# Performance work log

Hardware: AMD Instinct MI355X
Metric: run time of the kernel (lower is better)

## Reference

```python
import jax, jax.numpy as jnp
import numpy as np

B, N, D, H, M, CD = 2, 2048, 1024, 16, 77, 768
DH = D // H          # head dim 64
FF = 4 * D           # GEGLU hidden 4096
NBITS = 8
EPS = 1e-5


def fake_quant_w(w, n_bits=NBITS):
    """Per-tensor uniform affine INT8 fake-quant (UniformAffineQuantizerINT8) with STE."""
    levels = 2 ** n_bits - 1
    mn = jnp.min(w)
    mx = jnp.max(w)
    delta = (mx - mn) / levels
    zp = jnp.round(-mn / delta)
    wq = jnp.clip(jnp.round(w / delta) + zp, 0, levels)
    wdq = (wq - zp) * delta
    return w + jax.lax.stop_gradient(wdq - w)


def layernorm(x, g, b):
    mu = jnp.mean(x, axis=-1, keepdims=True)
    var = jnp.mean((x - mu) ** 2, axis=-1, keepdims=True)
    return (x - mu) * jax.lax.rsqrt(var + EPS) * g + b


def linear(x, w, b=None):
    y = x @ fake_quant_w(w).T
    return y if b is None else y + b


def cross_attn(x, ctx, qw, kw, vw, ow, ob):
    Bq, Nq, _ = x.shape
    Nk = ctx.shape[1]
    q = linear(x, qw).reshape(Bq, Nq, H, DH)     # b n h d
    k = linear(ctx, kw).reshape(Bq, Nk, H, DH)
    v = linear(ctx, vw).reshape(Bq, Nk, H, DH)
    scale = DH ** -0.5
    sim = jnp.einsum('bihd,bjhd->bhij', q, k) * scale   # [B,H,Nq,Nk]
    attn = jax.nn.softmax(sim, axis=-1)
    out = jnp.einsum('bhij,bjhd->bihd', attn, v).reshape(Bq, Nq, D)
    return linear(out, ow, ob)


def geglu_ff(x, w1, b1, w2, b2):
    h = linear(x, w1, b1)                # [B,N,2*FF]
    hidden, gate = jnp.split(h, 2, axis=-1)
    return linear(hidden * jax.nn.gelu(gate), w2, b2)


def setup_inputs() -> dict:
    key = jax.random.key(0)
    ks = jax.random.split(key, 24)
    W = lambda k, o, i: (jax.random.normal(k, (o, i), jnp.float32) * 0.02)
    return {
        'x': jax.random.normal(ks[0], (B, N, D), jnp.float32),
        'context': jax.random.normal(ks[1], (B, M, CD), jnp.float32),
        'ln1_g': 1.0 + 0.1 * jax.random.normal(ks[2], (D,), jnp.float32),
        'ln1_b': 0.1 * jax.random.normal(ks[3], (D,), jnp.float32),
        'ln2_g': 1.0 + 0.1 * jax.random.normal(ks[4], (D,), jnp.float32),
        'ln2_b': 0.1 * jax.random.normal(ks[5], (D,), jnp.float32),
        'ln3_g': 1.0 + 0.1 * jax.random.normal(ks[6], (D,), jnp.float32),
        'ln3_b': 0.1 * jax.random.normal(ks[7], (D,), jnp.float32),
        'q1_w': W(ks[8], D, D), 'k1_w': W(ks[9], D, D), 'v1_w': W(ks[10], D, D),
        'o1_w': W(ks[11], D, D), 'o1_b': jnp.zeros((D,), jnp.float32),
        'q2_w': W(ks[12], D, D), 'k2_w': W(ks[13], D, CD), 'v2_w': W(ks[14], D, CD),
        'o2_w': W(ks[15], D, D), 'o2_b': jnp.zeros((D,), jnp.float32),
        'ff1_w': W(ks[16], 2 * FF, D), 'ff1_b': jnp.zeros((2 * FF,), jnp.float32),
        'ff2_w': W(ks[17], D, FF), 'ff2_b': jnp.zeros((D,), jnp.float32),
    }


def reference(x, context, ln1_g, ln1_b, ln2_g, ln2_b, ln3_g, ln3_b,
              q1_w, k1_w, v1_w, o1_w, o1_b,
              q2_w, k2_w, v2_w, o2_w, o2_b,
              ff1_w, ff1_b, ff2_w, ff2_b):
    x = cross_attn(layernorm(x, ln1_g, ln1_b), layernorm(x, ln1_g, ln1_b),
                   q1_w, k1_w, v1_w, o1_w, o1_b) + x
    x = cross_attn(layernorm(x, ln2_g, ln2_b), context,
                   q2_w, k2_w, v2_w, o2_w, o2_b) + x
    x = geglu_ff(layernorm(x, ln3_g, ln3_b), ff1_w, ff1_b, ff2_w, ff2_b) + x
    return x
```

## Files before the change

kernel.cpp:

```cpp
#include <hip/hip_runtime.h>
#include <cstdint>
#include <cstddef>

typedef unsigned short ushort_t;
typedef short s16x8 __attribute__((ext_vector_type(8)));
typedef float f32x4 __attribute__((ext_vector_type(4)));
typedef unsigned u32x4 __attribute__((ext_vector_type(4)));

#define MFMA(A,B,C) __builtin_amdgcn_mfma_f32_16x16x32_bf16((A),(B),(C),0,0,0)

__device__ __forceinline__ float b2f(ushort_t h){ return __uint_as_float(((unsigned)h)<<16); }
__device__ __forceinline__ ushort_t f2b(float f){
  unsigned u = __float_as_uint(f);
  u += 0x7FFFu + ((u >> 16) & 1u);
  return (ushort_t)(u >> 16);
}
__device__ __forceinline__ unsigned f2o(float f){
  unsigned u = __float_as_uint(f);
  return (u & 0x80000000u) ? ~u : (u | 0x80000000u);
}
__device__ __forceinline__ float o2f(unsigned u){
  unsigned b = (u & 0x80000000u) ? (u & 0x7FFFFFFFu) : ~u;
  return __uint_as_float(b);
}

struct QT { const float* w[10]; ushort_t* o[10]; int n[10]; };

__global__ void init_k(unsigned* slots){
  int t = threadIdx.x;
  if (t < 20) slots[t] = (t & 1) ? 0u : 0xFFFFFFFFu;
}

__global__ __launch_bounds__(256) void minmax_k(QT qt, unsigned* slots){
  int t = blockIdx.y;
  const float4* w = (const float4*)qt.w[t];
  int n4 = qt.n[t] >> 2;
  float mn = 3.4e38f, mx = -3.4e38f;
  for (int i = blockIdx.x*256 + threadIdx.x; i < n4; i += gridDim.x*256){
    float4 v = w[i];
    mn = fminf(mn, fminf(fminf(v.x, v.y), fminf(v.z, v.w)));
    mx = fmaxf(mx, fmaxf(fmaxf(v.x, v.y), fmaxf(v.z, v.w)));
  }
  #pragma unroll
  for (int o = 1; o < 64; o <<= 1){
    mn = fminf(mn, __shfl_xor(mn, o));
    mx = fmaxf(mx, __shfl_xor(mx, o));
  }
  __shared__ float smn[4], smx[4];
  int wv = threadIdx.x >> 6;
  if ((threadIdx.x & 63) == 0){ smn[wv] = mn; smx[wv] = mx; }
  __syncthreads();
  if (threadIdx.x == 0){
    mn = fminf(fminf(smn[0], smn[1]), fminf(smn[2], smn[3]));
    mx = fmaxf(fmaxf(smx[0], smx[1]), fmaxf(smx[2], smx[3]));
    atomicMin(&slots[2*t], f2o(mn));
    atomicMax(&slots[2*t+1], f2o(mx));
  }
}

__global__ __launch_bounds__(256) void dequant_k(QT qt, const unsigned* __restrict__ slots){
  int t = blockIdx.y;
  float mn = o2f(slots[2*t]), mx = o2f(slots[2*t+1]);
  float delta = (mx - mn) * (1.f/255.f);
  float zp = rintf(-mn / delta);
  const float4* w = (const float4*)qt.w[t];
  ushort4* o = (ushort4*)qt.o[t];
  int n4 = qt.n[t] >> 2;
  for (int i = blockIdx.x*256 + threadIdx.x; i < n4; i += gridDim.x*256){
    float4 v = w[i];
    ushort4 r;
    float q;
    q = fminf(fmaxf(rintf(v.x/delta) + zp, 0.f), 255.f); r.x = f2b((q - zp)*delta);
    q = fminf(fmaxf(rintf(v.y/delta) + zp, 0.f), 255.f); r.y = f2b((q - zp)*delta);
    q = fminf(fmaxf(rintf(v.z/delta) + zp, 0.f), 255.f); r.z = f2b((q - zp)*delta);
    q = fminf(fmaxf(rintf(v.w/delta) + zp, 0.f), 255.f); r.w = f2b((q - zp)*delta);
    o[i] = r;
  }
}

__global__ __launch_bounds__(256) void f2b_k(const float* __restrict__ in, ushort_t* __restrict__ out, int n4){
  for (int i = blockIdx.x*256 + threadIdx.x; i < n4; i += gridDim.x*256){
    float4 v = ((const float4*)in)[i];
    ushort4 r; r.x = f2b(v.x); r.y = f2b(v.y); r.z = f2b(v.z); r.w = f2b(v.w);
    ((ushort4*)out)[i] = r;
  }
}

__global__ __launch_bounds__(256) void ln_k(const float* __restrict__ x, const float* __restrict__ g,
                                            const float* __restrict__ b, ushort_t* __restrict__ out){
  int row = blockIdx.x, tid = threadIdx.x;
  float4 v = ((const float4*)(x + (size_t)row*1024))[tid];
  float s  = v.x + v.y + v.z + v.w;
  float s2 = v.x*v.x + v.y*v.y + v.z*v.z + v.w*v.w;
  #pragma unroll
  for (int o = 1; o < 64; o <<= 1){ s += __shfl_xor(s, o); s2 += __shfl_xor(s2, o); }
  __shared__ float rs[4], rs2[4];
  int wv = tid >> 6;
  if ((tid & 63) == 0){ rs[wv] = s; rs2[wv] = s2; }
  __syncthreads();
  s = rs[0]+rs[1]+rs[2]+rs[3]; s2 = rs2[0]+rs2[1]+rs2[2]+rs2[3];
  float mu = s * (1.f/1024.f);
  float var = s2 * (1.f/1024.f) - mu*mu;
  float rstd = rsqrtf(var + 1e-5f);
  float4 gv = ((const float4*)g)[tid], bv = ((const float4*)b)[tid];
  ushort4 r;
  r.x = f2b((v.x - mu)*rstd*gv.x + bv.x);
  r.y = f2b((v.y - mu)*rstd*gv.y + bv.y);
  r.z = f2b((v.z - mu)*rstd*gv.z + bv.z);
  r.w = f2b((v.w - mu)*rstd*gv.w + bv.w);
  ((ushort4*)(out + (size_t)row*1024))[tid] = r;
}

__global__ __launch_bounds__(256) void gemm_k(
    const ushort_t* __restrict__ A, const ushort_t* __restrict__ W,
    const float* __restrict__ bias, const float* __restrict__ resid,
    float* __restrict__ outF, ushort_t* __restrict__ outB,
    int M, int N, int K, int lda, int ldw)
{
  __shared__ ushort_t As[3][128*32];
  __shared__ ushort_t Bs[3][128*32];
  const int tid = threadIdx.x;
  const int lane = tid & 63, wv = tid >> 6;
  const int g = lane >> 4, qi = lane & 15;

  const int gx = gridDim.x, gy = gridDim.y;
  const int lid = blockIdx.x + blockIdx.y * gx;
  const int w = gx >> 2, h = gy >> 1;
  const int xcd = lid & 7, o = lid >> 3;
  const int cx = xcd & 3, cy = xcd >> 2;
  const int n0 = (cx * w + (o % w)) * 128;
  const int m0 = (cy * h + (o / w)) * 128;

  const int koff = blockIdx.z * K;
  if (gridDim.z > 1) outF += (size_t)blockIdx.z * M * N;

  const int wr = (wv >> 1) * 64, wc = (wv & 1) * 64;
  f32x4 acc[4][4] = {};

  const int r0 = tid >> 2,        s0 = (tid & 3) ^ ((r0 >> 1) & 3);
  const int r1 = (256+tid) >> 2,  s1 = ((256+tid) & 3) ^ ((r1 >> 1) & 3);
  const int ar0 = (m0 + r0 < M) ? m0 + r0 : M - 1;
  const int ar1 = (m0 + r1 < M) ? m0 + r1 : M - 1;
  const size_t dst0 = (size_t)(wv*64)*8, dst1 = (size_t)(256 + wv*64)*8;

  #define GSTAGE(bi_, kt_) do {                                                    \
    __builtin_amdgcn_global_load_lds(                                              \
      (const __attribute__((address_space(1))) void*)(A + (size_t)ar0*lda + koff + (kt_) + s0*8), \
      (__attribute__((address_space(3))) void*)(&As[bi_][dst0]), 16, 0, 0);        \
    __builtin_amdgcn_global_load_lds(                                              \
      (const __attribute__((address_space(1))) void*)(W + (size_t)(n0 + r0)*ldw + koff + (kt_) + s0*8), \
      (__attribute__((address_space(3))) void*)(&Bs[bi_][dst0]), 16, 0, 0);        \
    __builtin_amdgcn_global_load_lds(                                              \
      (const __attribute__((address_space(1))) void*)(A + (size_t)ar1*lda + koff + (kt_) + s1*8), \
      (__attribute__((address_space(3))) void*)(&As[bi_][dst1]), 16, 0, 0);        \
    __builtin_amdgcn_global_load_lds(                                              \
      (const __attribute__((address_space(1))) void*)(W + (size_t)(n0 + r1)*ldw + koff + (kt_) + s1*8), \
      (__attribute__((address_space(3))) void*)(&Bs[bi_][dst1]), 16, 0, 0);        \
  } while(0)

  const int nt = K >> 5;
  GSTAGE(0, 0);
  if (nt > 1) GSTAGE(1, 32);
  if (nt > 1) asm volatile("s_waitcnt vmcnt(4)" ::: "memory");
  else        asm volatile("s_waitcnt vmcnt(0)" ::: "memory");
  __builtin_amdgcn_s_barrier();
  __builtin_amdgcn_sched_barrier(0);

  int bi = 0;
  for (int t = 0; t < nt; ++t){
    int b2 = bi + 2; if (b2 >= 3) b2 -= 3;
    if (t + 2 < nt) GSTAGE(b2, (t + 2) << 5);
    s16x8 af[4], bfr[4];
    #pragma unroll
    for (int mi = 0; mi < 4; ++mi){
      int row = wr + mi*16 + qi;
      int sl = g ^ ((row >> 1) & 3);
      af[mi] = *(const s16x8*)(&As[bi][row*32 + sl*8]);
    }
    #pragma unroll
    for (int ni = 0; ni < 4; ++ni){
      int row = wc + ni*16 + qi;
      int sl = g ^ ((row >> 1) & 3);
      bfr[ni] = *(const s16x8*)(&Bs[bi][row*32 + sl*8]);
    }
    __builtin_amdgcn_s_setprio(1);
    #pragma unroll
    for (int mi = 0; mi < 4; ++mi)
      #pragma unroll
      for (int ni = 0; ni < 4; ++ni)
        acc[mi][ni] = MFMA(af[mi], bfr[ni], acc[mi][ni]);
    __builtin_amdgcn_s_setprio(0);
    if (t + 1 < nt){
      if (t + 2 < nt) asm volatile("s_waitcnt vmcnt(4)" ::: "memory");
      else            asm volatile("s_waitcnt vmcnt(0)" ::: "memory");
      __builtin_amdgcn_s_barrier();
      __builtin_amdgcn_sched_barrier(0);
    }
    bi += 1; if (bi >= 3) bi -= 3;
  }
  #undef GSTAGE

  #pragma unroll
  for (int mi = 0; mi < 4; ++mi){
    #pragma unroll
    for (int r = 0; r < 4; ++r){
      int row = m0 + wr + mi*16 + g*4 + r;
      if (row >= M) continue;
      #pragma unroll
      for (int ni = 0; ni < 4; ++ni){
        int col = n0 + wc + ni*16 + qi;
        float v = acc[mi][ni][r];
        if (bias)  v += bias[col];
        if (resid) v += resid[(size_t)row*N + col];
        if (outF)  outF[(size_t)row*N + col] = v;
        else       outB[(size_t)row*N + col] = f2b(v);
      }
    }
  }
}

__global__ __launch_bounds__(256) void reduce_k(const float* __restrict__ p0, const float* __restrict__ p1,
                                                const float* __restrict__ bias, const float* __restrict__ resid,
                                                float* __restrict__ outF, ushort_t* __restrict__ outB, int n4){
  for (int i = blockIdx.x*256 + threadIdx.x; i < n4; i += gridDim.x*256){
    float4 a = ((const float4*)p0)[i];
    float4 b = ((const float4*)p1)[i];
    float4 v;
    v.x = a.x + b.x; v.y = a.y + b.y; v.z = a.z + b.z; v.w = a.w + b.w;
    if (bias){
      float4 bb = ((const float4*)bias)[i & 255];
      v.x += bb.x; v.y += bb.y; v.z += bb.z; v.w += bb.w;
    }
    if (resid){
      float4 r = ((const float4*)resid)[i];
      v.x += r.x; v.y += r.y; v.z += r.z; v.w += r.w;
    }
    if (outF) ((float4*)outF)[i] = v;
    else {
      ushort4 o; o.x = f2b(v.x); o.y = f2b(v.y); o.z = f2b(v.z); o.w = f2b(v.w);
      ((ushort4*)outB)[i] = o;
    }
  }
}

__global__ __launch_bounds__(256) void vtrans_k(const ushort_t* __restrict__ src, ushort_t* __restrict__ dst,
                                                int rows, int stride, int col_off, int nk_pad){
  __shared__ ushort_t ldst[64*130];
  int n0 = blockIdx.x * 128;
  int b = blockIdx.y >> 4, h = blockIdx.y & 15;
  const ushort_t* s = src + (size_t)b*rows*stride + col_off + h*64;
  for (int idx = threadIdx.x; idx < 128*64; idx += 256){
    int n = idx >> 6, d = idx & 63;
    int ng = n0 + n;
    ushort_t v = (ng < rows) ? s[(size_t)ng*stride + d] : (ushort_t)0;
    ldst[d*130 + n] = v;
  }
  __syncthreads();
  ushort_t* o = dst + (size_t)(b*16 + h)*64*nk_pad;
  for (int idx = threadIdx.x; idx < 64*128; idx += 256){
    int d = idx >> 7, n = idx & 127;
    if (n0 + n < nk_pad) o[(size_t)d*nk_pad + n0 + n] = ldst[d*130 + n];
  }
}

__global__ __launch_bounds__(256) void attn_k(
    const ushort_t* __restrict__ Q, const ushort_t* __restrict__ Kp, const ushort_t* __restrict__ Vt,
    ushort_t* __restrict__ O, int nq, int nk, int qstride, int kvstride, int nk_pad)
{
  __shared__ ushort_t Ks[2][32*64];
  __shared__ ushort_t Vs[2][64*32];
  const int tid = threadIdx.x, lane = tid & 63, wv = tid >> 6;
  const int g = lane >> 4, qi = lane & 15;
  const int b = blockIdx.y >> 4, h = blockIdx.y & 15;
  const int q0 = blockIdx.x*64 + wv*16;

  const ushort_t* Qr = Q + (size_t)(b*nq + q0 + qi)*qstride + h*64;
  s16x8 qf0 = *(const s16x8*)(Qr + g*8);
  s16x8 qf1 = *(const s16x8*)(Qr + 32 + g*8);
  const ushort_t* Kb = Kp + (size_t)b*nk*kvstride + h*64;
  const ushort_t* Vb = Vt + (size_t)(b*16 + h)*64*nk_pad;

  const int krow = wv*8 + (lane >> 3);
  const int kgsl = (lane & 7) ^ (krow & 7);
  const int vrow = wv*16 + (lane >> 2);
  const int vgsl = (lane & 3) ^ ((vrow >> 1) & 3);

  #define STAGE(buf, kb_) do {                                                   \
    int kr_ = (kb_) + krow; if (kr_ >= nk) kr_ = nk - 1;                         \
    __builtin_amdgcn_global_load_lds(                                            \
      (const __attribute__((address_space(1))) void*)(Kb + (size_t)kr_*kvstride + kgsl*8), \
      (__attribute__((address_space(3))) void*)(&Ks[buf][(size_t)wv*512]), 16, 0, 0); \
    __builtin_amdgcn_global_load_lds(                                            \
      (const __attribute__((address_space(1))) void*)(Vb + (size_t)vrow*nk_pad + (kb_) + vgsl*8), \
      (__attribute__((address_space(3))) void*)(&Vs[buf][(size_t)wv*512]), 16, 0, 0); \
  } while(0)

  const int nkp = (nk + 31) & ~31;
  f32x4 ot[4] = {};
  float m_run = -1e30f, l_run = 0.f;
  const float SC = 0.18033688011f;

  const int ks0 = (g     ^ (qi & 7)) * 8;
  const int ks1 = ((4+g) ^ (qi & 7)) * 8;
  const int vs0 = (g ^ ((qi >> 1) & 3)) * 8;

  STAGE(0, 0);
  asm volatile("s_waitcnt vmcnt(0)" ::: "memory");
  __syncthreads();
  int cur = 0;
  for (int kb = 0; kb < nkp; kb += 32){
    if (kb + 32 < nkp) STAGE(cur^1, kb + 32);
    s16x8 ka0 = *(const s16x8*)(&Ks[cur][(qi)*64      + ks0]);
    s16x8 ka1 = *(const s16x8*)(&Ks[cur][(qi)*64      + ks1]);
    s16x8 kb0 = *(const s16x8*)(&Ks[cur][(16+qi)*64   + ks0]);
    s16x8 kb1 = *(const s16x8*)(&Ks[cur][(16+qi)*64   + ks1]);
    s16x8 vf0 = *(const s16x8*)(&Vs[cur][(qi)*32      + vs0]);
    s16x8 vf1 = *(const s16x8*)(&Vs[cur][(16+qi)*32   + vs0]);
    s16x8 vf2 = *(const s16x8*)(&Vs[cur][(32+qi)*32   + vs0]);
    s16x8 vf3 = *(const s16x8*)(&Vs[cur][(48+qi)*32   + vs0]);

    f32x4 st0 = {}, st1 = {};
    st0 = MFMA(ka0, qf0, st0);
    st0 = MFMA(ka1, qf1, st0);
    st1 = MFMA(kb0, qf0, st1);
    st1 = MFMA(kb1, qf1, st1);
    float s[8];
    #pragma unroll
    for (int r = 0; r < 4; ++r){ s[r] = st0[r]*SC; s[4+r] = st1[r]*SC; }
    if (kb + 32 > nk){
      #pragma unroll
      for (int r = 0; r < 4; ++r){
        if (kb + 4*g + r >= nk)      s[r]   = -1e30f;
        if (kb + 16 + 4*g + r >= nk) s[4+r] = -1e30f;
      }
    }
    float bm = fmaxf(fmaxf(fmaxf(s[0], s[1]), fmaxf(s[2], s[3])),
                     fmaxf(fmaxf(s[4], s[5]), fmaxf(s[6], s[7])));
    bm = fmaxf(bm, __shfl_xor(bm, 16));
    bm = fmaxf(bm, __shfl_xor(bm, 32));
    if (!__all(bm <= m_run)){
      float m_new = fmaxf(m_run, bm);
      float fac = exp2f(m_run - m_new);
      l_run *= fac;
      #pragma unroll
      for (int dd = 0; dd < 4; ++dd)
        #pragma unroll
        for (int r = 0; r < 4; ++r) ot[dd][r] *= fac;
      m_run = m_new;
    }
    float p[8], rsum = 0.f;
    #pragma unroll
    for (int i = 0; i < 8; ++i){ p[i] = exp2f(s[i] - m_run); rsum += p[i]; }
    rsum += __shfl_xor(rsum, 16);
    rsum += __shfl_xor(rsum, 32);
    l_run += rsum;
    unsigned pk[4];
    #pragma unroll
    for (int r = 0; r < 4; ++r)
      pk[r] = (unsigned)f2b(p[r]) | ((unsigned)f2b(p[4+r]) << 16);
    int srcbase = ((2*g) & 3) * 16 + qi;
    unsigned sh0[4], sh1[4];
    #pragma unroll
    for (int r = 0; r < 4; ++r){
      sh0[r] = (unsigned)__shfl((int)pk[r], srcbase);
      sh1[r] = (unsigned)__shfl((int)pk[r], srcbase + 16);
    }
    unsigned sel = (g >> 1) ? 0x07060302u : 0x05040100u;
    u32x4 pw;
    pw[0] = __builtin_amdgcn_perm(sh0[1], sh0[0], sel);
    pw[1] = __builtin_amdgcn_perm(sh0[3], sh0[2], sel);
    pw[2] = __builtin_amdgcn_perm(sh1[1], sh1[0], sel);
    pw[3] = __builtin_amdgcn_perm(sh1[3], sh1[2], sel);
    s16x8 pf = __builtin_bit_cast(s16x8, pw);
    ot[0] = MFMA(vf0, pf, ot[0]);
    ot[1] = MFMA(vf1, pf, ot[1]);
    ot[2] = MFMA(vf2, pf, ot[2]);
    ot[3] = MFMA(vf3, pf, ot[3]);

    asm volatile("s_waitcnt vmcnt(0)" ::: "memory");
    __syncthreads();
    cur ^= 1;
  }
  #undef STAGE
  float inv = 1.f / l_run;
  ushort_t* Or = O + (size_t)(b*nq + q0 + qi)*1024 + h*64;
  #pragma unroll
  for (int dd = 0; dd < 4; ++dd)
    #pragma unroll
    for (int r = 0; r < 4; ++r)
      Or[dd*16 + 4*g + r] = f2b(ot[dd][r] * inv);
}

__global__ __launch_bounds__(256) void geglu_k(const ushort_t* __restrict__ h, ushort_t* __restrict__ out){
  int idx = blockIdx.x*256 + threadIdx.x;
  int r = idx >> 9, c = idx & 511;
  s16x8 hv = *(const s16x8*)(h + (size_t)r*8192 + c*8);
  s16x8 gv = *(const s16x8*)(h + (size_t)r*8192 + 4096 + c*8);
  s16x8 o;
  #pragma unroll
  for (int i = 0; i < 8; ++i){
    float gg = b2f((ushort_t)gv[i]);
    float t  = 0.7978845608f*(gg + 0.044715f*gg*gg*gg);
    float e  = __expf(2.f*t);
    float th = 1.f - 2.f/(e + 1.f);
    float ge = 0.5f*gg*(1.f + th);
    o[i] = (short)f2b(b2f((ushort_t)hv[i]) * ge);
  }
  *(s16x8*)(out + (size_t)r*4096 + c*8) = o;
}

extern "C" void kernel_launch(void* const* d_in, const int* in_sizes, int n_in,
                              void* d_out, int out_size, void* d_ws, size_t ws_size,
                              hipStream_t stream)
{
  const float* x    = (const float*)d_in[0];
  const float* ctx  = (const float*)d_in[1];
  const float* ln1g = (const float*)d_in[2];
  const float* ln1b = (const float*)d_in[3];
  const float* ln2g = (const float*)d_in[4];
  const float* ln2b = (const float*)d_in[5];
  const float* ln3g = (const float*)d_in[6];
  const float* ln3b = (const float*)d_in[7];
  const float* q1w  = (const float*)d_in[8];
  const float* k1w  = (const float*)d_in[9];
  const float* v1w  = (const float*)d_in[10];
  const float* o1w  = (const float*)d_in[11];
  const float* o1b  = (const float*)d_in[12];
  const float* q2w  = (const float*)d_in[13];
  const float* k2w  = (const float*)d_in[14];
  const float* v2w  = (const float*)d_in[15];
  const float* o2w  = (const float*)d_in[16];
  const float* o2b  = (const float*)d_in[17];
  const float* ff1w = (const float*)d_in[18];
  const float* ff1b = (const float*)d_in[19];
  const float* ff2w = (const float*)d_in[20];
  const float* ff2b = (const float*)d_in[21];

  char* base = (char*)d_ws;
  size_t off = 0;
  auto alloc = [&](size_t bytes) -> char* {
    char* p = base + off;
    off += (bytes + 255) & ~(size_t)255;
    return p;
  };
  unsigned*  slots = (unsigned*)alloc(80);
  ushort_t*  ctxb  = (ushort_t*)alloc((size_t)154*768*2);
  ushort_t*  wqkv1 = (ushort_t*)alloc((size_t)3072*1024*2);
  ushort_t*  o1d   = (ushort_t*)alloc((size_t)1024*1024*2);
  ushort_t*  q2d   = (ushort_t*)alloc((size_t)1024*1024*2);
  ushort_t*  wkv2  = (ushort_t*)alloc((size_t)2048*768*2);
  ushort_t*  o2d   = (ushort_t*)alloc((size_t)1024*1024*2);
  ushort_t*  f1d   = (ushort_t*)alloc((size_t)8192*1024*2);
  ushort_t*  f2d   = (ushort_t*)alloc((size_t)1024*4096*2);
  ushort_t*  lnb   = (ushort_t*)alloc((size_t)4096*1024*2);
  ushort_t*  qkvb  = (ushort_t*)alloc((size_t)4096*3072*2);
  ushort_t*  q2b   = (ushort_t*)alloc((size_t)4096*1024*2);
  ushort_t*  atb   = (ushort_t*)alloc((size_t)4096*1024*2);
  ushort_t*  kvb   = (ushort_t*)alloc((size_t)154*2048*2);
  ushort_t*  vt1   = (ushort_t*)alloc((size_t)2*16*64*2048*2);
  ushort_t*  vt2   = (ushort_t*)alloc((size_t)2*16*64*96*2);
  float*     x1    = (float*)alloc((size_t)4096*1024*4);
  float*     x2    = (float*)alloc((size_t)4096*1024*4);
  ushort_t*  hb    = (ushort_t*)alloc((size_t)4096*8192*2);
  ushort_t*  actb  = qkvb;
  float*     part  = (float*)hb;
  float*     part1 = part + (size_t)4096*1024;

  QT qt;
  qt.w[0]=q1w;  qt.o[0]=wqkv1;               qt.n[0]=1024*1024;
  qt.w[1]=k1w;  qt.o[1]=wqkv1+1024*1024;     qt.n[1]=1024*1024;
  qt.w[2]=v1w;  qt.o[2]=wqkv1+2*1024*1024;   qt.n[2]=1024*1024;
  qt.w[3]=o1w;  qt.o[3]=o1d;                 qt.n[3]=1024*1024;
  qt.w[4]=q2w;  qt.o[4]=q2d;                 qt.n[4]=1024*1024;
  qt.w[5]=k2w;  qt.o[5]=wkv2;                qt.n[5]=1024*768;
  qt.w[6]=v2w;  qt.o[6]=wkv2+1024*768;       qt.n[6]=1024*768;
  qt.w[7]=o2w;  qt.o[7]=o2d;                 qt.n[7]=1024*1024;
  qt.w[8]=ff1w; qt.o[8]=f1d;                 qt.n[8]=8192*1024;
  qt.w[9]=ff2w; qt.o[9]=f2d;                 qt.n[9]=1024*4096;

  init_k<<<1, 64, 0, stream>>>(slots);
  minmax_k<<<dim3(64,10), 256, 0, stream>>>(qt, slots);
  dequant_k<<<dim3(64,10), 256, 0, stream>>>(qt, slots);
  f2b_k<<<64, 256, 0, stream>>>(ctx, ctxb, 154*768/4);

  ln_k<<<4096, 256, 0, stream>>>(x, ln1g, ln1b, lnb);
  gemm_k<<<dim3(24, 32), 256, 0, stream>>>(lnb, wqkv1, nullptr, nullptr,
                                           nullptr, qkvb, 4096, 3072, 1024, 1024, 1024);
  vtrans_k<<<dim3(16, 32), 256, 0, stream>>>(qkvb, vt1, 2048, 3072, 2048, 2048);
  attn_k<<<dim3(32, 32), 256, 0, stream>>>(qkvb, qkvb+1024, vt1, atb,
                                           2048, 2048, 3072, 3072, 2048);
  gemm_k<<<dim3(8, 32, 2), 256, 0, stream>>>(atb, o1d, nullptr, nullptr,
                                             part, nullptr, 4096, 1024, 512, 1024, 1024);
  reduce_k<<<2048, 256, 0, stream>>>(part, part1, o1b, x, x1, nullptr, 4096*1024/4);

  ln_k<<<4096, 256, 0, stream>>>(x1, ln2g, ln2b, lnb);
  gemm_k<<<dim3(8, 32, 2), 256, 0, stream>>>(lnb, q2d, nullptr, nullptr,
                                             part, nullptr, 4096, 1024, 512, 1024, 1024);
  reduce_k<<<2048, 256, 0, stream>>>(part, part1, nullptr, nullptr, nullptr, q2b, 4096*1024/4);
  gemm_k<<<dim3(16, 2), 256, 0, stream>>>(ctxb, wkv2, nullptr, nullptr,
                                          nullptr, kvb, 154, 2048, 768, 768, 768);
  vtrans_k<<<dim3(1, 32), 256, 0, stream>>>(kvb, vt2, 77, 2048, 1024, 96);
  attn_k<<<dim3(32, 32), 256, 0, stream>>>(q2b, kvb, vt2, atb,
                                           2048, 77, 1024, 2048, 96);
  gemm_k<<<dim3(8, 32, 2), 256, 0, stream>>>(atb, o2d, nullptr, nullptr,
                                             part, nullptr, 4096, 1024, 512, 1024, 1024);
  reduce_k<<<2048, 256, 0, stream>>>(part, part1, o2b, x1, x2, nullptr, 4096*1024/4);

  ln_k<<<4096, 256, 0, stream>>>(x2, ln3g, ln3b, lnb);
  gemm_k<<<dim3(64, 32), 256, 0, stream>>>(lnb, f1d, ff1b, nullptr,
                                           nullptr, hb, 4096, 8192, 1024, 1024, 1024);
  geglu_k<<<8192, 256, 0, stream>>>(hb, actb);
  gemm_k<<<dim3(8, 32, 2), 256, 0, stream>>>(actb, f2d, nullptr, nullptr,
                                             part, nullptr, 4096, 1024, 2048, 4096, 4096);
  reduce_k<<<2048, 256, 0, stream>>>(part, part1, ff2b, x2,
                                     (float*)d_out, nullptr, 4096*1024/4);
}
```

Measured before the change: 646.8 us.

## Enlarge GEMM tile to 256x128 with 512-thread blocks

Changes the GEMM kernel to use 8 waves per block and a 256-row A tile (256x128 output tile), so each loaded W tile is reused across twice as many rows. The staging loads are rebalanced to two A loads and one B load per thread, and the vmcnt waits are adjusted. The XCD-aware block swizzle gets a fallback when grid dimensions are not divisible, and all launches halve grid.y. This trades higher LDS use per block and fewer blocks (a worse wave count for some GEMMs, e.g. the small KV GEMM) for better reuse of W loads.

```diff
diff --git a/kernel.cpp b/kernel.cpp
--- a/kernel.cpp
+++ b/kernel.cpp
@@ -111,13 +111,13 @@
   ((ushort4*)(out + (size_t)row*1024))[tid] = r;
 }
 
-__global__ __launch_bounds__(256) void gemm_k(
+__global__ __launch_bounds__(512) void gemm_k(
     const ushort_t* __restrict__ A, const ushort_t* __restrict__ W,
     const float* __restrict__ bias, const float* __restrict__ resid,
     float* __restrict__ outF, ushort_t* __restrict__ outB,
     int M, int N, int K, int lda, int ldw)
 {
-  __shared__ ushort_t As[3][128*32];
+  __shared__ ushort_t As[3][256*32];
   __shared__ ushort_t Bs[3][128*32];
   const int tid = threadIdx.x;
   const int lane = tid & 63, wv = tid >> 6;
@@ -125,11 +125,17 @@
 
   const int gx = gridDim.x, gy = gridDim.y;
   const int lid = blockIdx.x + blockIdx.y * gx;
-  const int w = gx >> 2, h = gy >> 1;
-  const int xcd = lid & 7, o = lid >> 3;
-  const int cx = xcd & 3, cy = xcd >> 2;
-  const int n0 = (cx * w + (o % w)) * 128;
-  const int m0 = (cy * h + (o / w)) * 128;
+  int m0, n0;
+  if (((gx & 3) | (gy & 1)) == 0){
+    const int w = gx >> 2, h = gy >> 1;
+    const int xcd = lid & 7, o = lid >> 3;
+    const int cx = xcd & 3, cy = xcd >> 2;
+    n0 = (cx * w + (o % w)) * 128;
+    m0 = (cy * h + (o / w)) * 256;
+  } else {
+    n0 = blockIdx.x * 128;
+    m0 = blockIdx.y * 256;
+  }
 
   const int koff = blockIdx.z * K;
   if (gridDim.z > 1) outF += (size_t)blockIdx.z * M * N;
@@ -137,31 +143,28 @@
   const int wr = (wv >> 1) * 64, wc = (wv & 1) * 64;
   f32x4 acc[4][4] = {};
 
-  const int r0 = tid >> 2,        s0 = (tid & 3) ^ ((r0 >> 1) & 3);
-  const int r1 = (256+tid) >> 2,  s1 = ((256+tid) & 3) ^ ((r1 >> 1) & 3);
-  const int ar0 = (m0 + r0 < M) ? m0 + r0 : M - 1;
-  const int ar1 = (m0 + r1 < M) ? m0 + r1 : M - 1;
-  const size_t dst0 = (size_t)(wv*64)*8, dst1 = (size_t)(256 + wv*64)*8;
+  const int ra0 = tid >> 2,        sa0 = (tid & 3) ^ ((ra0 >> 1) & 3);
+  const int ra1 = (512+tid) >> 2,  sa1 = ((512+tid) & 3) ^ ((ra1 >> 1) & 3);
+  const int aA0 = (m0 + ra0 < M) ? m0 + ra0 : M - 1;
+  const int aA1 = (m0 + ra1 < M) ? m0 + ra1 : M - 1;
+  const size_t dA0 = (size_t)tid*8, dA1 = (size_t)(512+tid)*8, dB0 = (size_t)tid*8;
 
   #define GSTAGE(bi_, kt_) do {                                                    \
     __builtin_amdgcn_global_load_lds(                                              \
-      (const __attribute__((address_space(1))) void*)(A + (size_t)ar0*lda + koff + (kt_) + s0*8), \
-      (__attribute__((address_space(3))) void*)(&As[bi_][dst0]), 16, 0, 0);        \
+      (const __attribute__((address_space(1))) void*)(A + (size_t)aA0*lda + koff + (kt_) + sa0*8), \
+      (__attribute__((address_space(3))) void*)(&As[bi_][dA0]), 16, 0, 0);         \
     __builtin_amdgcn_global_load_lds(                                              \
-      (const __attribute__((address_space(1))) void*)(W + (size_t)(n0 + r0)*ldw + koff + (kt_) + s0*8), \
-      (__attribute__((address_space(3))) void*)(&Bs[bi_][dst0]), 16, 0, 0);        \
+      (const __attribute__((address_space(1))) void*)(A + (size_t)aA1*lda + koff + (kt_) + sa1*8), \
+      (__attribute__((address_space(3))) void*)(&As[bi_][dA1]), 16, 0, 0);         \
     __builtin_amdgcn_global_load_lds(                                              \
-      (const __attribute__((address_space(1))) void*)(A + (size_t)ar1*lda + koff + (kt_) + s1*8), \
-      (__attribute__((address_space(3))) void*)(&As[bi_][dst1]), 16, 0, 0);        \
-    __builtin_amdgcn_global_load_lds(                                              \
-      (const __attribute__((address_space(1))) void*)(W + (size_t)(n0 + r1)*ldw + koff + (kt_) + s1*8), \
-      (__attribute__((address_space(3))) void*)(&Bs[bi_][dst1]), 16, 0, 0);        \
+      (const __attribute__((address_space(1))) void*)(W + (size_t)(n0 + ra0)*ldw + koff + (kt_) + sa0*8), \
+      (__attribute__((address_space(3))) void*)(&Bs[bi_][dB0]), 16, 0, 0);         \
   } while(0)
 
   const int nt = K >> 5;
   GSTAGE(0, 0);
   if (nt > 1) GSTAGE(1, 32);
-  if (nt > 1) asm volatile("s_waitcnt vmcnt(4)" ::: "memory");
+  if (nt > 1) asm volatile("s_waitcnt vmcnt(3)" ::: "memory");
   else        asm volatile("s_waitcnt vmcnt(0)" ::: "memory");
   __builtin_amdgcn_s_barrier();
   __builtin_amdgcn_sched_barrier(0);
@@ -191,7 +194,7 @@
         acc[mi][ni] = MFMA(af[mi], bfr[ni], acc[mi][ni]);
     __builtin_amdgcn_s_setprio(0);
     if (t + 1 < nt){
-      if (t + 2 < nt) asm volatile("s_waitcnt vmcnt(4)" ::: "memory");
+      if (t + 2 < nt) asm volatile("s_waitcnt vmcnt(3)" ::: "memory");
       else            asm volatile("s_waitcnt vmcnt(0)" ::: "memory");
       __builtin_amdgcn_s_barrier();
       __builtin_amdgcn_sched_barrier(0);
@@ -484,33 +487,33 @@
   f2b_k<<<64, 256, 0, stream>>>(ctx, ctxb, 154*768/4);
 
   ln_k<<<4096, 256, 0, stream>>>(x, ln1g, ln1b, lnb);
-  gemm_k<<<dim3(24, 32), 256, 0, stream>>>(lnb, wqkv1, nullptr, nullptr,
+  gemm_k<<<dim3(24, 16), 512, 0, stream>>>(lnb, wqkv1, nullptr, nullptr,
                                            nullptr, qkvb, 4096, 3072, 1024, 1024, 1024);
   vtrans_k<<<dim3(16, 32), 256, 0, stream>>>(qkvb, vt1, 2048, 3072, 2048, 2048);
   attn_k<<<dim3(32, 32), 256, 0, stream>>>(qkvb, qkvb+1024, vt1, atb,
                                            2048, 2048, 3072, 3072, 2048);
-  gemm_k<<<dim3(8, 32, 2), 256, 0, stream>>>(atb, o1d, nullptr, nullptr,
+  gemm_k<<<dim3(8, 16, 2), 512, 0, stream>>>(atb, o1d, nullptr, nullptr,
                                              part, nullptr, 4096, 1024, 512, 1024, 1024);
   reduce_k<<<2048, 256, 0, stream>>>(part, part1, o1b, x, x1, nullptr, 4096*1024/4);
 
   ln_k<<<4096, 256, 0, stream>>>(x1, ln2g, ln2b, lnb);
-  gemm_k<<<dim3(8, 32, 2), 256, 0, stream>>>(lnb, q2d, nullptr, nullptr,
+  gemm_k<<<dim3(8, 16, 2), 512, 0, stream>>>(lnb, q2d, nullptr, nullptr,
                                              part, nullptr, 4096, 1024, 512, 1024, 1024);
   reduce_k<<<2048, 256, 0, stream>>>(part, part1, nullptr, nullptr, nullptr, q2b, 4096*1024/4);
-  gemm_k<<<dim3(16, 2), 256, 0, stream>>>(ctxb, wkv2, nullptr, nullptr,
+  gemm_k<<<dim3(16, 1), 512, 0, stream>>>(ctxb, wkv2, nullptr, nullptr,
                                           nullptr, kvb, 154, 2048, 768, 768, 768);
   vtrans_k<<<dim3(1, 32), 256, 0, stream>>>(kvb, vt2, 77, 2048, 1024, 96);
   attn_k<<<dim3(32, 32), 256, 0, stream>>>(q2b, kvb, vt2, atb,
                                            2048, 77, 1024, 2048, 96);
-  gemm_k<<<dim3(8, 32, 2), 256, 0, stream>>>(atb, o2d, nullptr, nullptr,
+  gemm_k<<<dim3(8, 16, 2), 512, 0, stream>>>(atb, o2d, nullptr, nullptr,
                                              part, nullptr, 4096, 1024, 512, 1024, 1024);
   reduce_k<<<2048, 256, 0, stream>>>(part, part1, o2b, x1, x2, nullptr, 4096*1024/4);
 
   ln_k<<<4096, 256, 0, stream>>>(x2, ln3g, ln3b, lnb);
-  gemm_k<<<dim3(64, 32), 256, 0, stream>>>(lnb, f1d, ff1b, nullptr,
+  gemm_k<<<dim3(64, 16), 512, 0, stream>>>(lnb, f1d, ff1b, nullptr,
                                            nullptr, hb, 4096, 8192, 1024, 1024, 1024);
   geglu_k<<<8192, 256, 0, stream>>>(hb, actb);
-  gemm_k<<<dim3(8, 32, 2), 256, 0, stream>>>(actb, f2d, nullptr, nullptr,
+  gemm_k<<<dim3(8, 16, 2), 512, 0, stream>>>(actb, f2d, nullptr, nullptr,
                                              part, nullptr, 4096, 1024, 2048, 4096, 4096);
   reduce_k<<<2048, 256, 0, stream>>>(part, part1, ff2b, x2,
                                      (float*)d_out, nullptr, 4096*1024/4);
```

New measurement: 633.2 us. 2.1% less time.
